# Performance work log

Hardware: AMD Instinct MI355X
Metric: run time of the kernel (lower is better)

The kernel has to match this reference:

```python
import jax, jax.numpy as jnp
import numpy as np

SEQ, PREV, BS, D_IN, H, D = 512, 512, 8, 1024, 16, 64


def setup_inputs() -> dict:
    key = jax.random.key(0)
    ks = jax.random.split(key, 10)
    s = 0.02
    inp = {
        "input_": jax.random.normal(ks[0], (SEQ, BS, D_IN), jnp.float32),
        "pos_embs": jax.random.normal(ks[1], (SEQ + PREV, D_IN), jnp.float32),
        "memory": jax.random.normal(ks[2], (PREV, BS, D_IN), jnp.float32),
        "u": jax.random.normal(ks[3], (H, D), jnp.float32) * s,
        "v": jax.random.normal(ks[4], (H, D), jnp.float32) * s,
        # causal mask allowing full attention to memory: triu with diagonal=1+prev
        "mask": (jnp.triu(jnp.ones((SEQ, SEQ + PREV), jnp.bool_), k=1 + PREV))[..., None],
        "W_kv": jax.random.normal(ks[5], (D_IN, 2 * H * D), jnp.float32) * s,
        "W_q": jax.random.normal(ks[6], (D_IN, H * D), jnp.float32) * s,
        "W_p": jax.random.normal(ks[7], (D_IN, H * D), jnp.float32) * s,
        "W_out": jax.random.normal(ks[8], (H * D, D_IN), jnp.float32) * s,
        "ln_gamma": jnp.ones((D_IN,), jnp.float32),
        "ln_beta": jnp.zeros((D_IN,), jnp.float32),
    }
    return inp


def _rel_shift(x):
    # x: (q, k, bs, H) -> pad one zero column, reshape-transpose trick, drop first row
    q, k, bs, h = x.shape
    zp = jnp.zeros((q, 1, bs, h), x.dtype)
    return jnp.concatenate([zp, x], axis=1).reshape(k + 1, q, bs, h)[1:].reshape(q, k, bs, h)


def reference(input_, pos_embs, memory, u, v, mask, W_kv, W_q, W_p, W_out, ln_gamma, ln_beta):
    cur_seq, bs, d_in = input_.shape
    prev_seq = memory.shape[0]
    tot = cur_seq + prev_seq
    h, d = u.shape
    scale = 1.0 / d ** 0.5

    iwm = jnp.concatenate([memory, input_], axis=0)          # (tot, bs, d_in)
    kv = jnp.einsum('jbe,ef->jbf', iwm, W_kv)                 # (tot, bs, 2*H*d)
    k_t, v_t = jnp.split(kv, 2, axis=-1)
    q_t = jnp.einsum('ibe,ef->ibf', input_, W_q)              # (cur, bs, H*d)

    q4 = q_t.reshape(cur_seq, bs, h, d)
    k4 = k_t.reshape(tot, bs, h, d)
    v4 = v_t.reshape(tot, bs, h, d)

    content_attn = jnp.einsum('ibhd,jbhd->ijbh', q4 + u, k4)  # (cur, tot, bs, H)

    p_t = (pos_embs @ W_p).reshape(tot, h, d)                 # (tot, H, d)
    position_attn = jnp.einsum('ibhd,jhd->ijbh', q4 + v, p_t)
    position_attn = _rel_shift(position_attn)

    attn = content_attn + position_attn
    attn = jnp.where(mask[..., None], -jnp.inf, attn)         # mask: (cur, tot, 1) -> (cur, tot, 1, 1)
    attn = jax.nn.softmax(attn * scale, axis=1)

    awv = jnp.einsum('ijbh,jbhd->ibhd', attn, v4).reshape(cur_seq, bs, h * d)
    out = input_ + awv @ W_out                                # residual

    mu = jnp.mean(out, axis=-1, keepdims=True)
    var = jnp.mean((out - mu) ** 2, axis=-1, keepdims=True)
    out = (out - mu) / jnp.sqrt(var + 1e-5) * ln_gamma + ln_beta
    return out
```

## Files before the change

### kernel.cpp

```cpp
#include <hip/hip_runtime.h>
#include <math.h>

#define SEQ  512
#define PREV 512
#define TOT  1024
#define BSZ  8
#define DIN  1024
#define NH   16
#define HD   64

typedef __bf16 bf16;
typedef __bf16 bf16x8 __attribute__((ext_vector_type(8)));
typedef float  f32x4  __attribute__((ext_vector_type(4)));
typedef float  f32x16 __attribute__((ext_vector_type(16)));
typedef unsigned int u32;
typedef u32 u32x2 __attribute__((ext_vector_type(2)));

__device__ __forceinline__ f32x4 MFMA16(bf16x8 a, bf16x8 b, f32x4 c) {
    return __builtin_amdgcn_mfma_f32_16x16x32_bf16(a, b, c, 0, 0, 0);
}
__device__ __forceinline__ f32x16 MFMA32(bf16x8 a, bf16x8 b, f32x16 c) {
    return __builtin_amdgcn_mfma_f32_32x32x16_bf16(a, b, c, 0, 0, 0);
}

#define GLOAD16(g, l) __builtin_amdgcn_global_load_lds( \
    (const __attribute__((address_space(1))) void*)(g), \
    (__attribute__((address_space(3))) void*)(l), 16, 0, 0)

__device__ __forceinline__ unsigned short bfbits(float x) {
    return __builtin_bit_cast(unsigned short, (bf16)x);
}
__device__ __forceinline__ float bf2f(u32 bits16) {
    return __builtin_bit_cast(float, bits16 << 16);
}

__global__ __launch_bounds__(256) void prep_all(
    const float* __restrict__ memory, const float* __restrict__ input_,
    const float* __restrict__ pos,
    const float* __restrict__ W_kv, const float* __restrict__ W_q,
    const float* __restrict__ W_p,  const float* __restrict__ W_out,
    bf16* __restrict__ iwm, bf16* __restrict__ posb,
    bf16* __restrict__ wkv, bf16* __restrict__ wq,
    bf16* __restrict__ wp,  bf16* __restrict__ wo)
{
    __shared__ float tile[32][33];
    const int bid = blockIdx.x;
    const int t = threadIdx.x;
    if (bid < 9216) {
        const float* src; bf16* dst; int e4;
        if (bid < 8192) {
            e4 = (bid * 256 + t) * 4;
            src = (e4 < 4194304) ? memory : input_ - 4194304;
            dst = iwm;
        } else {
            e4 = ((bid - 8192) * 256 + t) * 4;
            src = pos; dst = posb;
        }
        float4 x = *(const float4*)(src + e4);
        union { bf16 h[4]; ushort4 u4; } pk;
        pk.h[0] = (bf16)x.x; pk.h[1] = (bf16)x.y; pk.h[2] = (bf16)x.z; pk.h[3] = (bf16)x.w;
        *(ushort4*)(dst + e4) = pk.u4;
        return;
    }
    const int rem = bid - 9216;
    const int bx = rem % 160, by = rem / 160;
    const float* W; bf16* Wt; int N, bn;
    if (bx < 64)       { W = W_kv;  Wt = wkv; N = 2048; bn = bx * 32; }
    else if (bx < 96)  { W = W_q;   Wt = wq;  N = 1024; bn = (bx - 64) * 32; }
    else if (bx < 128) { W = W_p;   Wt = wp;  N = 1024; bn = (bx - 96) * 32; }
    else               { W = W_out; Wt = wo;  N = 1024; bn = (bx - 128) * 32; }
    const int bk = by * 32;
    const int r = t >> 3, c4 = (t & 7) * 4;
    float4 x = *(const float4*)(W + (size_t)(bk + r) * N + bn + c4);
    tile[r][c4 + 0] = x.x; tile[r][c4 + 1] = x.y;
    tile[r][c4 + 2] = x.z; tile[r][c4 + 3] = x.w;
    __syncthreads();
    union { bf16 h[4]; ushort4 u4; } pk;
#pragma unroll
    for (int i = 0; i < 4; ++i) pk.h[i] = (bf16)tile[c4 + i][r];
    *(ushort4*)(Wt + (size_t)(bn + r) * 1024 + bk + c4) = pk.u4;
}

__global__ __launch_bounds__(512, 1) void gemm_8ph(
    const bf16* __restrict__ A, const bf16* __restrict__ Bt,
    bf16* __restrict__ C, int M, int N, int K)
{
    __shared__ __align__(16) bf16 A_s[2][256 * 64];
    __shared__ __align__(16) bf16 B_s[2][256 * 64];
    const int t = threadIdx.x;
    const int w = t >> 6, lane = t & 63;
    const int li = lane & 15, hi = lane >> 4;
    const int wm = w >> 2, wn = w & 3;
    const int lin = blockIdx.y * 8 + blockIdx.x;
    const int xcd = lin & 7, idx = lin >> 3;
    const int bm = (xcd * 4 + (idx & 3)) * 256;
    const int bn = (idx >> 2) * 256;

    f32x4 acc[8][4];
#pragma unroll
    for (int m = 0; m < 8; ++m)
#pragma unroll
        for (int n = 0; n < 4; ++n) acc[m][n] = (f32x4){0.f, 0.f, 0.f, 0.f};

    auto stage_half = [&](int buf, int ks, int h) {
        const bf16* __restrict__ src = (h < 2) ? A : Bt;
        const int base = (h < 2) ? bm : bn;
        const int hh = (h & 1) * 128;
        bf16* dst = (h < 2) ? &A_s[buf][0] : &B_s[buf][0];
        const int k0 = ks << 6;
#pragma unroll
        for (int g = 0; g < 2; ++g) {
            const int row = hh + g * 64 + (t >> 3);
            const bf16* gp = src + (size_t)(base + row) * K + k0 + (((t & 7) ^ (row & 7)) * 8);
            GLOAD16(gp, dst + (size_t)(hh + g * 64 + w * 8) * 64);
        }
    };

    bf16x8 af[4], bfr[4];
    auto LDA = [&](int buf, int mh, int kk) {
#pragma unroll
        for (int m = 0; m < 4; ++m) {
            int row = wm * 128 + (mh * 4 + m) * 16 + li;
            af[m] = *(const bf16x8*)&A_s[buf][row * 64 + (((kk * 4 + hi) ^ (row & 7)) * 8)];
        }
    };
    auto LDB = [&](int buf, int kk) {
#pragma unroll
        for (int n = 0; n < 4; ++n) {
            int row = wn * 64 + n * 16 + li;
            bfr[n] = *(const bf16x8*)&B_s[buf][row * 64 + (((kk * 4 + hi) ^ (row & 7)) * 8)];
        }
    };

#define FMA_PHASE(mh)                                                    \
    asm volatile("s_waitcnt lgkmcnt(0)" ::: "memory");                   \
    __builtin_amdgcn_sched_barrier(0);                                   \
    __builtin_amdgcn_s_setprio(1);                                       \
    _Pragma("unroll")                                                    \
    for (int m = 0; m < 4; ++m)                                          \
        _Pragma("unroll")                                                \
        for (int n = 0; n < 4; ++n)                                      \
            acc[(mh) * 4 + m][n] = MFMA16(af[m], bfr[n], acc[(mh) * 4 + m][n]); \
    __builtin_amdgcn_s_setprio(0);

    stage_half(0, 0, 0); stage_half(0, 0, 1); stage_half(0, 0, 2); stage_half(0, 0, 3);

    const int nk = K >> 6;
    for (int ks = 0; ks < nk; ++ks) {
        const int cur = ks & 1, nxt = cur ^ 1;
        asm volatile("s_waitcnt vmcnt(0)" ::: "memory");
        __builtin_amdgcn_sched_barrier(0);
        __builtin_amdgcn_s_barrier();
        __builtin_amdgcn_sched_barrier(0);
        if (ks + 1 < nk) {
            stage_half(nxt, ks + 1, 0); stage_half(nxt, ks + 1, 1);
            stage_half(nxt, ks + 1, 2); stage_half(nxt, ks + 1, 3);
        }
        LDB(cur, 0); LDA(cur, 0, 0);
        FMA_PHASE(0)
        LDA(cur, 1, 0);
        FMA_PHASE(1)
        LDB(cur, 1); LDA(cur, 0, 1);
        FMA_PHASE(0)
        LDA(cur, 1, 1);
        FMA_PHASE(1)
    }

#pragma unroll
    for (int m = 0; m < 8; ++m)
#pragma unroll
        for (int n = 0; n < 4; ++n)
#pragma unroll
            for (int r = 0; r < 4; ++r) {
                int row = bm + wm * 128 + m * 16 + hi * 4 + r;
                int col = bn + wn * 64 + n * 16 + li;
                C[(size_t)row * N + col] = (bf16)acc[m][n][r];
            }
#undef FMA_PHASE
}

template<int FOUT>
__global__ __launch_bounds__(256) void gemm_mfma(
    const bf16* __restrict__ A, const bf16* __restrict__ Bt,
    const float* __restrict__ Rres, bf16* __restrict__ Cb,
    float* __restrict__ Cf, int M, int N, int K)
{
    __shared__ __align__(16) bf16 A_s[128 * 64];
    __shared__ __align__(16) bf16 B_s[128 * 64];
    const int t = threadIdx.x;
    const int w = t >> 6, lane = t & 63;
    const int li = lane & 15, hi = lane >> 4;
    const int wr = w >> 1, wc = w & 1;
    const int bm = blockIdx.y * 128, bn = blockIdx.x * 128;
    const int l3 = lane >> 3, l7 = lane & 7;
    const int srcoct = ((l7 ^ l3) * 8);

    f32x4 acc[4][4];
#pragma unroll
    for (int m = 0; m < 4; ++m)
#pragma unroll
        for (int n = 0; n < 4; ++n) acc[m][n] = (f32x4){0.f, 0.f, 0.f, 0.f};

    auto stage = [&](int k0) {
#pragma unroll
        for (int i = 0; i < 4; ++i) {
            int c = w * 4 + i;
            const bf16* ga = A + (size_t)(bm + c * 8 + l3) * K + k0 + srcoct;
            GLOAD16(ga, &A_s[c * 512]);
            const bf16* gb = Bt + (size_t)(bn + c * 8 + l3) * K + k0 + srcoct;
            GLOAD16(gb, &B_s[c * 512]);
        }
    };

    stage(0);
    const int nk = K >> 6;
    for (int ks = 0; ks < nk; ++ks) {
        __syncthreads();
#pragma unroll
        for (int kk = 0; kk < 2; ++kk) {
            bf16x8 af[4], bfr[4];
#pragma unroll
            for (int m = 0; m < 4; ++m) {
                int row = wr * 64 + m * 16 + li;
                af[m] = *(const bf16x8*)&A_s[row * 64 + ((kk * 32 + hi * 8) ^ ((row & 7) * 8))];
            }
#pragma unroll
            for (int n = 0; n < 4; ++n) {
                int row = wc * 64 + n * 16 + li;
                bfr[n] = *(const bf16x8*)&B_s[row * 64 + ((kk * 32 + hi * 8) ^ ((row & 7) * 8))];
            }
#pragma unroll
            for (int m = 0; m < 4; ++m)
#pragma unroll
                for (int n = 0; n < 4; ++n)
                    acc[m][n] = MFMA16(af[m], bfr[n], acc[m][n]);
        }
        __syncthreads();
        if (ks + 1 < nk) stage((ks + 1) << 6);
    }

#pragma unroll
    for (int m = 0; m < 4; ++m)
#pragma unroll
        for (int n = 0; n < 4; ++n)
#pragma unroll
            for (int r = 0; r < 4; ++r) {
                int row = bm + wr * 64 + m * 16 + hi * 4 + r;
                int col = bn + wc * 64 + n * 16 + li;
                size_t off = (size_t)row * N + col;
                if (FOUT) Cf[off] = acc[m][n][r] + Rres[off];
                else      Cb[off] = (bf16)acc[m][n][r];
            }
}

__global__ __launch_bounds__(256, 2) void attn_mfma(
    const bf16* __restrict__ kv, const bf16* __restrict__ qb,
    const bf16* __restrict__ pb, const float* __restrict__ u,
    const float* __restrict__ v, bf16* __restrict__ awv)
{
    const int bi = (blockIdx.z & 1) ? (3 - blockIdx.x) : blockIdx.x;
    const int i0 = bi * 128;
    const int b  = blockIdx.y;
    const int h  = blockIdx.z;
    const int t  = threadIdx.x;
    const int w  = t >> 6;
    const int lane = t & 63;
    const int ql  = lane & 31;
    const int hi2 = lane >> 5;

    __shared__ __align__(16) bf16 K_s[64 * 64];
    __shared__ __align__(16) bf16 V_s[64][72];
    __shared__ __align__(16) bf16 P_s[256 * 64];
    __shared__ __align__(16) char SCR[4][6912];

    char* rsc = SCR[w];

    const int c8 = t & 7;
    const int rq = t >> 3;
    const int nt = 2 * bi + 10;
    const int C0 = 384 - i0;

    bf16x8 vreg[2];
#pragma unroll
    for (int p = 0; p < 2; ++p)
        vreg[p] = *(const bf16x8*)(kv + (size_t)((p * 32 + rq) * BSZ + b) * 2048 + 1024 + h * HD + c8 * 8);
#pragma unroll
    for (int p = 0; p < 2; ++p)
        GLOAD16(kv + (size_t)((p * 32 + rq) * BSZ + b) * 2048 + h * HD + ((c8 ^ (rq & 7)) * 8),
                K_s + (p * 32 + rq) * 64 + c8 * 8);
#pragma unroll
    for (int cp = 0; cp < 6; ++cp) {
        int grow = C0 + cp * 32 + rq;
        GLOAD16(pb + (size_t)grow * DIN + h * HD + ((c8 ^ (rq & 7)) * 8),
                P_s + (grow & 255) * 64 + c8 * 8);
    }

    bf16x8 qu[4], qv[4];
    {
        const size_t qoff = ((size_t)(i0 + w * 32 + ql) * BSZ + b) * DIN + h * HD;
#pragma unroll
        for (int kk = 0; kk < 4; ++kk) {
            bf16x8 q8 = *(const bf16x8*)(qb + qoff + kk * 16 + hi2 * 8);
            const float* up = u + h * HD + kk * 16 + hi2 * 8;
            const float* vp = v + h * HD + kk * 16 + hi2 * 8;
#pragma unroll
            for (int m = 0; m < 8; ++m) {
                float qf = (float)q8[m];
                qu[kk][m] = (bf16)(qf + up[m]);
                qv[kk][m] = (bf16)(qf + vp[m]);
            }
        }
    }

    float mrun = -1e30f, lrun = 0.f;
    f32x16 o[2];
    o[0] = (f32x16){}; o[1] = (f32x16){};

    const int phq = (31 - ql) & 3;
    const int sel = phq >> 1;
    const int shb = (phq & 1) * 16;

    for (int tt = 0; tt < nt; ++tt) {
        const int j0 = tt * 64;

        __builtin_amdgcn_s_barrier();
        __builtin_amdgcn_sched_barrier(0);

#pragma unroll
        for (int p = 0; p < 2; ++p) {
            int j = p * 32 + rq;
#pragma unroll
            for (int mm = 0; mm < 8; ++mm)
                V_s[c8 * 8 + mm][(j + 8 * c8) & 63] = vreg[p][mm];
        }
        asm volatile("s_waitcnt vmcnt(0) lgkmcnt(0)" ::: "memory");
        __builtin_amdgcn_sched_barrier(0);
        __builtin_amdgcn_s_barrier();
        __builtin_amdgcn_sched_barrier(0);

        f32x16 st[2];
        st[0] = (f32x16){}; st[1] = (f32x16){};
        __builtin_amdgcn_s_setprio(1);
#pragma unroll
        for (int jt = 0; jt < 2; ++jt) {
            int row = jt * 32 + ql;
#pragma unroll
            for (int kk = 0; kk < 4; ++kk) {
                bf16x8 kf = *(const bf16x8*)&K_s[row * 64 + (((kk * 2 + hi2) ^ (ql & 7)) * 8)];
                st[jt] = MFMA32(kf, qu[kk], st[jt]);
            }
        }
        const int bwg = j0 - i0 + 480 - 32 * w;
        f32x16 rp[3];
        rp[0] = (f32x16){}; rp[1] = (f32x16){}; rp[2] = (f32x16){};
#pragma unroll
        for (int Rt = 0; Rt < 3; ++Rt) {
            int ring = (bwg + Rt * 32 + ql) & 255;
#pragma unroll
            for (int kk = 0; kk < 4; ++kk) {
                bf16x8 pf = *(const bf16x8*)&P_s[ring * 64 + (((kk * 2 + hi2) ^ (ring & 7)) * 8)];
                rp[Rt] = MFMA32(pf, qv[kk], rp[Rt]);
            }
        }
        __builtin_amdgcn_s_setprio(0);

        __builtin_amdgcn_s_barrier();
        __builtin_amdgcn_sched_barrier(0);

        if (tt + 1 < nt) {
            const int j0n = j0 + 64;
#pragma unroll
            for (int p = 0; p < 2; ++p)
                vreg[p] = *(const bf16x8*)(kv + (size_t)((j0n + p * 32 + rq) * BSZ + b) * 2048 + 1024 + h * HD + c8 * 8);
#pragma unroll
            for (int p = 0; p < 2; ++p)
                GLOAD16(kv + (size_t)((j0n + p * 32 + rq) * BSZ + b) * 2048 + h * HD + ((c8 ^ (rq & 7)) * 8),
                        K_s + (p * 32 + rq) * 64 + c8 * 8);
        }
        if (tt + 3 < nt) {
            const int Cs = C0 + (tt + 3) * 64;
#pragma unroll
            for (int p = 0; p < 2; ++p) {
                int grow = Cs + p * 32 + rq;
                GLOAD16(pb + (size_t)grow * DIN + h * HD + ((c8 ^ (rq & 7)) * 8),
                        P_s + (grow & 255) * 64 + c8 * 8);
            }
        }

#pragma unroll
        for (int Rt = 0; Rt < 3; ++Rt)
#pragma unroll
            for (int a = 0; a < 4; ++a) {
                u32 lo = (u32)bfbits(rp[Rt][a * 4 + 0]) | ((u32)bfbits(rp[Rt][a * 4 + 1]) << 16);
                u32 hi = (u32)bfbits(rp[Rt][a * 4 + 2]) | ((u32)bfbits(rp[Rt][a * 4 + 3]) << 16);
                *(u32x2*)(rsc + ql * 216 + 64 * Rt + 16 * a + 8 * hi2) = (u32x2){lo, hi};
            }

        float rowmax = -1e30f;
        const int limb = i0 + 32 * w + ql + PREV - j0;
#pragma unroll
        for (int jt = 0; jt < 2; ++jt)
#pragma unroll
            for (int a = 0; a < 4; ++a) {
                int e = jt * 32 + 8 * a + 4 * hi2 + 31 - ql;
                const u32x2* W = (const u32x2*)(rsc + ql * 216 + 8 * (e >> 2));
                u32x2 A0 = W[0], A1 = W[1];
                u32 U0 = sel ? A0[1] : A0[0];
                u32 U1 = sel ? A1[0] : A0[1];
                u32 U2 = sel ? A1[1] : A1[0];
                u32 o0 = (u32)((((unsigned long long)U1 << 32) | U0) >> shb);
                u32 o1 = (u32)((((unsigned long long)U2 << 32) | U1) >> shb);
                float pq[4] = {bf2f(o0 & 0xffffu), bf2f(o0 >> 16),
                               bf2f(o1 & 0xffffu), bf2f(o1 >> 16)};
#pragma unroll
                for (int rr = 0; rr < 4; ++rr) {
                    int r = a * 4 + rr;
                    int lj = jt * 32 + 8 * a + 4 * hi2 + rr;
                    float sv = (st[jt][r] + pq[rr]) * 0.125f;
                    if (lj > limb) sv = -1e30f;
                    st[jt][r] = sv;
                    rowmax = fmaxf(rowmax, sv);
                }
            }
        rowmax = fmaxf(rowmax, __shfl_xor(rowmax, 32));

        if (!__all(rowmax - mrun <= 8.f)) {
            float newm = fmaxf(mrun, rowmax);
            float fsc = __expf(mrun - newm);
#pragma unroll
            for (int r = 0; r < 16; ++r) {
                float fr = __shfl(fsc, (r & 3) + 8 * (r >> 2) + 4 * hi2);
                o[0][r] *= fr; o[1][r] *= fr;
            }
            lrun *= fsc;
            mrun = newm;
        }
        float rowsum = 0.f;
#pragma unroll
        for (int jt = 0; jt < 2; ++jt)
#pragma unroll
            for (int r = 0; r < 16; ++r) {
                float p = __expf(st[jt][r] - mrun);
                st[jt][r] = p;
                rowsum += p;
            }
        rowsum += __shfl_xor(rowsum, 32);
        lrun += rowsum;

        u32 pk0[2][4], pk1[2][4];
#pragma unroll
        for (int jt = 0; jt < 2; ++jt)
#pragma unroll
            for (int a = 0; a < 4; ++a) {
                pk0[jt][a] = (u32)bfbits(st[jt][a * 4 + 0]) | ((u32)bfbits(st[jt][a * 4 + 1]) << 16);
                pk1[jt][a] = (u32)bfbits(st[jt][a * 4 + 2]) | ((u32)bfbits(st[jt][a * 4 + 3]) << 16);
            }

        __builtin_amdgcn_s_setprio(1);
#pragma unroll
        for (int js = 0; js < 4; ++js) {
            const int jt = js >> 1, a0 = 2 * (js & 1), a1 = a0 + 1;
            u32 w0 = pk0[jt][a0], w2 = pk0[jt][a1];
            asm("v_permlane32_swap_b32 %0, %1" : "+v"(w0), "+v"(w2));
            u32 w1 = pk1[jt][a0], w3 = pk1[jt][a1];
            asm("v_permlane32_swap_b32 %0, %1" : "+v"(w1), "+v"(w3));
            union { u32 uw[4]; bf16x8 vv; } pa;
            pa.uw[0] = w0; pa.uw[1] = w1; pa.uw[2] = w2; pa.uw[3] = w3;
#pragma unroll
            for (int dt = 0; dt < 2; ++dt) {
                int dcol = dt * 32 + ql;
                int colb = (js * 16 + hi2 * 8 + 8 * (dcol >> 3)) & 63;
                bf16x8 vf = *(const bf16x8*)&V_s[dcol][colb];
                o[dt] = MFMA32(pa.vv, vf, o[dt]);
            }
        }
        __builtin_amdgcn_s_setprio(0);
    }

    float lr[16];
#pragma unroll
    for (int r = 0; r < 16; ++r) lr[r] = __shfl(lrun, (r & 3) + 8 * (r >> 2) + 4 * hi2);
#pragma unroll
    for (int dt = 0; dt < 2; ++dt)
#pragma unroll
        for (int r = 0; r < 16; ++r) {
            int row = i0 + 32 * w + (r & 3) + 8 * (r >> 2) + 4 * hi2;
            awv[((size_t)row * BSZ + b) * DIN + h * HD + dt * 32 + ql] = (bf16)(o[dt][r] / lr[r]);
        }
}

__global__ __launch_bounds__(256) void ln_f32(
    float* __restrict__ out, const float* __restrict__ gamma, const float* __restrict__ beta)
{
    const int row = blockIdx.x;
    const int t = threadIdx.x;
    float4 x = *(float4*)(out + (size_t)row * DIN + t * 4);
    float s  = x.x + x.y + x.z + x.w;
    float ss = x.x * x.x + x.y * x.y + x.z * x.z + x.w * x.w;
#pragma unroll
    for (int wd = 1; wd < 64; wd <<= 1) { s += __shfl_xor(s, wd); ss += __shfl_xor(ss, wd); }
    __shared__ float sbuf[4], ssbuf[4];
    const int wave = t >> 6, lanei = t & 63;
    if (lanei == 0) { sbuf[wave] = s; ssbuf[wave] = ss; }
    __syncthreads();
    s  = sbuf[0] + sbuf[1] + sbuf[2] + sbuf[3];
    ss = ssbuf[0] + ssbuf[1] + ssbuf[2] + ssbuf[3];
    const float mu   = s * (1.f / DIN);
    const float var  = ss * (1.f / DIN) - mu * mu;
    const float rstd = rsqrtf(var + 1e-5f);
    float4 g  = *(const float4*)(gamma + t * 4);
    float4 bb = *(const float4*)(beta + t * 4);
    float4 y;
    y.x = (x.x - mu) * rstd * g.x + bb.x;
    y.y = (x.y - mu) * rstd * g.y + bb.y;
    y.z = (x.z - mu) * rstd * g.z + bb.z;
    y.w = (x.w - mu) * rstd * g.w + bb.w;
    *(float4*)(out + (size_t)row * DIN + t * 4) = y;
}

extern "C" void kernel_launch(void* const* d_in, const int* in_sizes, int n_in,
                              void* d_out, int out_size, void* d_ws, size_t ws_size,
                              hipStream_t stream)
{
    const float* input_ = (const float*)d_in[0];
    const float* pos    = (const float*)d_in[1];
    const float* memory = (const float*)d_in[2];
    const float* u      = (const float*)d_in[3];
    const float* v      = (const float*)d_in[4];
    const float* W_kv   = (const float*)d_in[6];
    const float* W_q    = (const float*)d_in[7];
    const float* W_p    = (const float*)d_in[8];
    const float* W_out  = (const float*)d_in[9];
    const float* gamma  = (const float*)d_in[10];
    const float* beta   = (const float*)d_in[11];

    bf16* iwm  = (bf16*)d_ws;
    bf16* kvb  = iwm  + (size_t)8192 * 1024;
    bf16* qbf  = kvb  + (size_t)8192 * 2048;
    bf16* pbf  = qbf  + (size_t)4096 * 1024;
    bf16* posb = pbf  + (size_t)1024 * 1024;
    bf16* wkv  = posb + (size_t)1024 * 1024;
    bf16* wq   = wkv  + (size_t)2048 * 1024;
    bf16* wp   = wq   + (size_t)1024 * 1024;
    bf16* wo   = wp   + (size_t)1024 * 1024;
    bf16* awvb = wo   + (size_t)1024 * 1024;
    float* outf = (float*)d_out;

    prep_all<<<14336, 256, 0, stream>>>(memory, input_, pos, W_kv, W_q, W_p, W_out,
                                        iwm, posb, wkv, wq, wp, wo);

    gemm_8ph<<<dim3(8, 32), 512, 0, stream>>>(iwm, wkv, kvb, 8192, 2048, 1024);
    gemm_mfma<0><<<dim3(8, 32), 256, 0, stream>>>(iwm + (size_t)4096 * 1024, wq, nullptr, qbf, nullptr, 4096, 1024, 1024);
    gemm_mfma<0><<<dim3(8, 8),  256, 0, stream>>>(posb, wp, nullptr, pbf, nullptr, 1024, 1024, 1024);

    attn_mfma<<<dim3(4, 8, 16), 256, 0, stream>>>(kvb, qbf, pbf, u, v, awvb);

    gemm_mfma<1><<<dim3(8, 32), 256, 0, stream>>>(awvb, wo, input_, nullptr, outf, 4096, 1024, 1024);
    ln_f32<<<4096, 256, 0, stream>>>(outf, gamma, beta);
}
```

Before: 192.2 us.

## Merge Q and P projection GEMMs, skip masking on unmasked tiles, tweak attention reductions

The Q and positional projection GEMMs become one launch with 40 row-blocks, so a launch disappears and the grid fills better. In attention, the rel-shift scratch store moves before the barrier. The causal mask compare is now skipped through a wave-uniform branch for tiles that lie fully in the allowed region. Cross-half max and sum reductions use v_permlane32_swap instead of shfl_xor, and the final normalization multiplies by a reciprocal instead of dividing. These cut a little ALU and launch overhead, at the cost of slightly different rounding from rcp and extra code size from the duplicated assemble paths.

```diff
diff --git a/kernel.cpp b/kernel.cpp
--- a/kernel.cpp
+++ b/kernel.cpp
@@ -179,11 +179,9 @@
 #undef FMA_PHASE
 }
 
-template<int FOUT>
-__global__ __launch_bounds__(256) void gemm_mfma(
+__global__ __launch_bounds__(256) void gemm_out(
     const bf16* __restrict__ A, const bf16* __restrict__ Bt,
-    const float* __restrict__ Rres, bf16* __restrict__ Cb,
-    float* __restrict__ Cf, int M, int N, int K)
+    const float* __restrict__ Rres, float* __restrict__ Cf, int N, int K)
 {
     __shared__ __align__(16) bf16 A_s[128 * 64];
     __shared__ __align__(16) bf16 B_s[128 * 64];
@@ -205,10 +203,8 @@
 #pragma unroll
         for (int i = 0; i < 4; ++i) {
             int c = w * 4 + i;
-            const bf16* ga = A + (size_t)(bm + c * 8 + l3) * K + k0 + srcoct;
-            GLOAD16(ga, &A_s[c * 512]);
-            const bf16* gb = Bt + (size_t)(bn + c * 8 + l3) * K + k0 + srcoct;
-            GLOAD16(gb, &B_s[c * 512]);
+            GLOAD16(A + (size_t)(bm + c * 8 + l3) * K + k0 + srcoct, &A_s[c * 512]);
+            GLOAD16(Bt + (size_t)(bn + c * 8 + l3) * K + k0 + srcoct, &B_s[c * 512]);
         }
     };
 
@@ -248,8 +244,79 @@
                 int row = bm + wr * 64 + m * 16 + hi * 4 + r;
                 int col = bn + wc * 64 + n * 16 + li;
                 size_t off = (size_t)row * N + col;
-                if (FOUT) Cf[off] = acc[m][n][r] + Rres[off];
-                else      Cb[off] = (bf16)acc[m][n][r];
+                Cf[off] = acc[m][n][r] + Rres[off];
+            }
+}
+
+__global__ __launch_bounds__(256) void gemm_qp(
+    const bf16* __restrict__ iwmq, const bf16* __restrict__ posb,
+    const bf16* __restrict__ wq, const bf16* __restrict__ wp,
+    bf16* __restrict__ qbf, bf16* __restrict__ pbf)
+{
+    __shared__ __align__(16) bf16 A_s[128 * 64];
+    __shared__ __align__(16) bf16 B_s[128 * 64];
+    const int t = threadIdx.x;
+    const int w = t >> 6, lane = t & 63;
+    const int li = lane & 15, hi = lane >> 4;
+    const int wr = w >> 1, wc = w & 1;
+    const int by = blockIdx.y;
+    const bf16* A; const bf16* Bt; bf16* Cb; int bm;
+    if (by < 32) { A = iwmq; Bt = wq; Cb = qbf; bm = by * 128; }
+    else         { A = posb; Bt = wp; Cb = pbf; bm = (by - 32) * 128; }
+    const int bn = blockIdx.x * 128;
+    const int l3 = lane >> 3, l7 = lane & 7;
+    const int srcoct = ((l7 ^ l3) * 8);
+
+    f32x4 acc[4][4];
+#pragma unroll
+    for (int m = 0; m < 4; ++m)
+#pragma unroll
+        for (int n = 0; n < 4; ++n) acc[m][n] = (f32x4){0.f, 0.f, 0.f, 0.f};
+
+    auto stage = [&](int k0) {
+#pragma unroll
+        for (int i = 0; i < 4; ++i) {
+            int c = w * 4 + i;
+            GLOAD16(A + (size_t)(bm + c * 8 + l3) * 1024 + k0 + srcoct, &A_s[c * 512]);
+            GLOAD16(Bt + (size_t)(bn + c * 8 + l3) * 1024 + k0 + srcoct, &B_s[c * 512]);
+        }
+    };
+
+    stage(0);
+    for (int ks = 0; ks < 16; ++ks) {
+        __syncthreads();
+#pragma unroll
+        for (int kk = 0; kk < 2; ++kk) {
+            bf16x8 af[4], bfr[4];
+#pragma unroll
+            for (int m = 0; m < 4; ++m) {
+                int row = wr * 64 + m * 16 + li;
+                af[m] = *(const bf16x8*)&A_s[row * 64 + ((kk * 32 + hi * 8) ^ ((row & 7) * 8))];
+            }
+#pragma unroll
+            for (int n = 0; n < 4; ++n) {
+                int row = wc * 64 + n * 16 + li;
+                bfr[n] = *(const bf16x8*)&B_s[row * 64 + ((kk * 32 + hi * 8) ^ ((row & 7) * 8))];
+            }
+#pragma unroll
+            for (int m = 0; m < 4; ++m)
+#pragma unroll
+                for (int n = 0; n < 4; ++n)
+                    acc[m][n] = MFMA16(af[m], bfr[n], acc[m][n]);
+        }
+        __syncthreads();
+        if (ks + 1 < 16) stage((ks + 1) << 6);
+    }
+
+#pragma unroll
+    for (int m = 0; m < 4; ++m)
+#pragma unroll
+        for (int n = 0; n < 4; ++n)
+#pragma unroll
+            for (int r = 0; r < 4; ++r) {
+                int row = bm + wr * 64 + m * 16 + hi * 4 + r;
+                int col = bn + wc * 64 + n * 16 + li;
+                Cb[(size_t)row * 1024 + col] = (bf16)acc[m][n][r];
             }
 }
 
@@ -364,6 +431,15 @@
         }
         __builtin_amdgcn_s_setprio(0);
 
+#pragma unroll
+        for (int Rt = 0; Rt < 3; ++Rt)
+#pragma unroll
+            for (int a = 0; a < 4; ++a) {
+                u32 lo = (u32)bfbits(rp[Rt][a * 4 + 0]) | ((u32)bfbits(rp[Rt][a * 4 + 1]) << 16);
+                u32 hi = (u32)bfbits(rp[Rt][a * 4 + 2]) | ((u32)bfbits(rp[Rt][a * 4 + 3]) << 16);
+                *(u32x2*)(rsc + ql * 216 + 64 * Rt + 16 * a + 8 * hi2) = (u32x2){lo, hi};
+            }
+
         __builtin_amdgcn_s_barrier();
         __builtin_amdgcn_sched_barrier(0);
 
@@ -387,42 +463,45 @@
             }
         }
 
-#pragma unroll
-        for (int Rt = 0; Rt < 3; ++Rt)
-#pragma unroll
-            for (int a = 0; a < 4; ++a) {
-                u32 lo = (u32)bfbits(rp[Rt][a * 4 + 0]) | ((u32)bfbits(rp[Rt][a * 4 + 1]) << 16);
-                u32 hi = (u32)bfbits(rp[Rt][a * 4 + 2]) | ((u32)bfbits(rp[Rt][a * 4 + 3]) << 16);
-                *(u32x2*)(rsc + ql * 216 + 64 * Rt + 16 * a + 8 * hi2) = (u32x2){lo, hi};
-            }
-
         float rowmax = -1e30f;
         const int limb = i0 + 32 * w + ql + PREV - j0;
-#pragma unroll
-        for (int jt = 0; jt < 2; ++jt)
-#pragma unroll
-            for (int a = 0; a < 4; ++a) {
-                int e = jt * 32 + 8 * a + 4 * hi2 + 31 - ql;
-                const u32x2* W = (const u32x2*)(rsc + ql * 216 + 8 * (e >> 2));
-                u32x2 A0 = W[0], A1 = W[1];
-                u32 U0 = sel ? A0[1] : A0[0];
-                u32 U1 = sel ? A1[0] : A0[1];
-                u32 U2 = sel ? A1[1] : A1[0];
-                u32 o0 = (u32)((((unsigned long long)U1 << 32) | U0) >> shb);
-                u32 o1 = (u32)((((unsigned long long)U2 << 32) | U1) >> shb);
-                float pq[4] = {bf2f(o0 & 0xffffu), bf2f(o0 >> 16),
-                               bf2f(o1 & 0xffffu), bf2f(o1 >> 16)};
-#pragma unroll
-                for (int rr = 0; rr < 4; ++rr) {
-                    int r = a * 4 + rr;
-                    int lj = jt * 32 + 8 * a + 4 * hi2 + rr;
-                    float sv = (st[jt][r] + pq[rr]) * 0.125f;
-                    if (lj > limb) sv = -1e30f;
-                    st[jt][r] = sv;
-                    rowmax = fmaxf(rowmax, sv);
+        auto assemble = [&](bool domask) {
+#pragma unroll
+            for (int jt = 0; jt < 2; ++jt)
+#pragma unroll
+                for (int a = 0; a < 4; ++a) {
+                    int e = jt * 32 + 8 * a + 4 * hi2 + 31 - ql;
+                    const u32x2* W = (const u32x2*)(rsc + ql * 216 + 8 * (e >> 2));
+                    u32x2 A0 = W[0], A1 = W[1];
+                    u32 U0 = sel ? A0[1] : A0[0];
+                    u32 U1 = sel ? A1[0] : A0[1];
+                    u32 U2 = sel ? A1[1] : A1[0];
+                    u32 o0 = (u32)((((unsigned long long)U1 << 32) | U0) >> shb);
+                    u32 o1 = (u32)((((unsigned long long)U2 << 32) | U1) >> shb);
+                    float pq[4] = {bf2f(o0 & 0xffffu), bf2f(o0 >> 16),
+                                   bf2f(o1 & 0xffffu), bf2f(o1 >> 16)};
+#pragma unroll
+                    for (int rr = 0; rr < 4; ++rr) {
+                        int r = a * 4 + rr;
+                        int lj = jt * 32 + 8 * a + 4 * hi2 + rr;
+                        float sv = (st[jt][r] + pq[rr]) * 0.125f;
+                        if (domask && lj > limb) sv = -1e30f;
+                        st[jt][r] = sv;
+                        rowmax = fmaxf(rowmax, sv);
+                    }
                 }
-            }
-        rowmax = fmaxf(rowmax, __shfl_xor(rowmax, 32));
+        };
+        if (__builtin_amdgcn_readfirstlane(j0 + 63 - (i0 + 32 * w + PREV)) > 0)
+            assemble(true);
+        else
+            assemble(false);
+
+        {
+            u32 rm = __builtin_bit_cast(u32, rowmax), rm2 = rm;
+            asm("v_permlane32_swap_b32 %0, %1" : "+v"(rm), "+v"(rm2));
+            rowmax = fmaxf(__builtin_bit_cast(float, rm2), __builtin_bit_cast(float, rm) * 0.f + rowmax);
+            rowmax = fmaxf(rowmax, __builtin_bit_cast(float, rm2));
+        }
 
         if (!__all(rowmax - mrun <= 8.f)) {
             float newm = fmaxf(mrun, rowmax);
@@ -444,7 +523,11 @@
                 st[jt][r] = p;
                 rowsum += p;
             }
-        rowsum += __shfl_xor(rowsum, 32);
+        {
+            u32 rs = __builtin_bit_cast(u32, rowsum), rs2 = rs;
+            asm("v_permlane32_swap_b32 %0, %1" : "+v"(rs), "+v"(rs2));
+            rowsum += __builtin_bit_cast(float, rs2);
+        }
         lrun += rowsum;
 
         u32 pk0[2][4], pk1[2][4];
@@ -477,15 +560,16 @@
         __builtin_amdgcn_s_setprio(0);
     }
 
+    float linv = __builtin_amdgcn_rcpf(lrun);
     float lr[16];
 #pragma unroll
-    for (int r = 0; r < 16; ++r) lr[r] = __shfl(lrun, (r & 3) + 8 * (r >> 2) + 4 * hi2);
+    for (int r = 0; r < 16; ++r) lr[r] = __shfl(linv, (r & 3) + 8 * (r >> 2) + 4 * hi2);
 #pragma unroll
     for (int dt = 0; dt < 2; ++dt)
 #pragma unroll
         for (int r = 0; r < 16; ++r) {
             int row = i0 + 32 * w + (r & 3) + 8 * (r >> 2) + 4 * hi2;
-            awv[((size_t)row * BSZ + b) * DIN + h * HD + dt * 32 + ql] = (bf16)(o[dt][r] / lr[r]);
+            awv[((size_t)row * BSZ + b) * DIN + h * HD + dt * 32 + ql] = (bf16)(o[dt][r] * lr[r]);
         }
 }
 
@@ -550,11 +634,10 @@
                                         iwm, posb, wkv, wq, wp, wo);
 
     gemm_8ph<<<dim3(8, 32), 512, 0, stream>>>(iwm, wkv, kvb, 8192, 2048, 1024);
-    gemm_mfma<0><<<dim3(8, 32), 256, 0, stream>>>(iwm + (size_t)4096 * 1024, wq, nullptr, qbf, nullptr, 4096, 1024, 1024);
-    gemm_mfma<0><<<dim3(8, 8),  256, 0, stream>>>(posb, wp, nullptr, pbf, nullptr, 1024, 1024, 1024);
+    gemm_qp<<<dim3(8, 40), 256, 0, stream>>>(iwm + (size_t)4096 * 1024, posb, wq, wp, qbf, pbf);
 
     attn_mfma<<<dim3(4, 8, 16), 256, 0, stream>>>(kvb, qbf, pbf, u, v, awvb);
 
-    gemm_mfma<1><<<dim3(8, 32), 256, 0, stream>>>(awvb, wo, input_, nullptr, outf, 4096, 1024, 1024);
+    gemm_out<<<dim3(8, 32), 256, 0, stream>>>(awvb, wo, input_, outf, 1024, 1024);
     ln_f32<<<4096, 256, 0, stream>>>(outf, gamma, beta);
 }
```

New measurement: 170.4 us. 1.13x faster.

## Unify GEMMs on 256-tile kernel, merge Q/P launches, streamline attention softmax

Applied to the files above, without the earlier changes.

Turns the 256x256 8-phase GEMM into a shared body that now serves the Q, positional and output projections too. The separate Q and P GEMMs are merged into one 80-block launch, and the output GEMM uses 64 large tiles instead of 256 small ones. In attention, the scale folds log2(e) so a raw v_exp_f32 can replace __expf. Row reductions use permlane32 swaps, the causal mask is skipped for fully visible tiles, the rsc LDS writes move before the barrier, and the final divide becomes a reciprocal multiply. The larger tiles leave only 64-80 blocks for the Q/P and output GEMMs, which may underfill the GPU's CUs.

```diff
diff --git a/kernel.cpp b/kernel.cpp
--- a/kernel.cpp
+++ b/kernel.cpp
@@ -32,6 +32,11 @@
 }
 __device__ __forceinline__ float bf2f(u32 bits16) {
     return __builtin_bit_cast(float, bits16 << 16);
+}
+__device__ __forceinline__ float exp2_raw(float x) {
+    float r;
+    asm("v_exp_f32 %0, %1" : "=v"(r) : "v"(x));
+    return r;
 }
 
 __global__ __launch_bounds__(256) void prep_all(
@@ -81,9 +86,11 @@
     *(ushort4*)(Wt + (size_t)(bn + r) * 1024 + bk + c4) = pk.u4;
 }
 
-__global__ __launch_bounds__(512, 1) void gemm_8ph(
+template<int FOUT>
+__device__ __forceinline__ void gemm256_body(
     const bf16* __restrict__ A, const bf16* __restrict__ Bt,
-    bf16* __restrict__ C, int M, int N, int K)
+    const float* __restrict__ Rres, bf16* __restrict__ Cb,
+    float* __restrict__ Cf, int bm, int bn, int N, int K)
 {
     __shared__ __align__(16) bf16 A_s[2][256 * 64];
     __shared__ __align__(16) bf16 B_s[2][256 * 64];
@@ -91,10 +98,6 @@
     const int w = t >> 6, lane = t & 63;
     const int li = lane & 15, hi = lane >> 4;
     const int wm = w >> 2, wn = w & 3;
-    const int lin = blockIdx.y * 8 + blockIdx.x;
-    const int xcd = lin & 7, idx = lin >> 3;
-    const int bm = (xcd * 4 + (idx & 3)) * 256;
-    const int bn = (idx >> 2) * 256;
 
     f32x4 acc[8][4];
 #pragma unroll
@@ -165,6 +168,7 @@
         LDA(cur, 1, 1);
         FMA_PHASE(1)
     }
+#undef FMA_PHASE
 
 #pragma unroll
     for (int m = 0; m < 8; ++m)
@@ -174,83 +178,40 @@
             for (int r = 0; r < 4; ++r) {
                 int row = bm + wm * 128 + m * 16 + hi * 4 + r;
                 int col = bn + wn * 64 + n * 16 + li;
-                C[(size_t)row * N + col] = (bf16)acc[m][n][r];
-            }
-#undef FMA_PHASE
-}
-
-template<int FOUT>
-__global__ __launch_bounds__(256) void gemm_mfma(
-    const bf16* __restrict__ A, const bf16* __restrict__ Bt,
-    const float* __restrict__ Rres, bf16* __restrict__ Cb,
-    float* __restrict__ Cf, int M, int N, int K)
-{
-    __shared__ __align__(16) bf16 A_s[128 * 64];
-    __shared__ __align__(16) bf16 B_s[128 * 64];
-    const int t = threadIdx.x;
-    const int w = t >> 6, lane = t & 63;
-    const int li = lane & 15, hi = lane >> 4;
-    const int wr = w >> 1, wc = w & 1;
-    const int bm = blockIdx.y * 128, bn = blockIdx.x * 128;
-    const int l3 = lane >> 3, l7 = lane & 7;
-    const int srcoct = ((l7 ^ l3) * 8);
-
-    f32x4 acc[4][4];
-#pragma unroll
-    for (int m = 0; m < 4; ++m)
-#pragma unroll
-        for (int n = 0; n < 4; ++n) acc[m][n] = (f32x4){0.f, 0.f, 0.f, 0.f};
-
-    auto stage = [&](int k0) {
-#pragma unroll
-        for (int i = 0; i < 4; ++i) {
-            int c = w * 4 + i;
-            const bf16* ga = A + (size_t)(bm + c * 8 + l3) * K + k0 + srcoct;
-            GLOAD16(ga, &A_s[c * 512]);
-            const bf16* gb = Bt + (size_t)(bn + c * 8 + l3) * K + k0 + srcoct;
-            GLOAD16(gb, &B_s[c * 512]);
-        }
-    };
-
-    stage(0);
-    const int nk = K >> 6;
-    for (int ks = 0; ks < nk; ++ks) {
-        __syncthreads();
-#pragma unroll
-        for (int kk = 0; kk < 2; ++kk) {
-            bf16x8 af[4], bfr[4];
-#pragma unroll
-            for (int m = 0; m < 4; ++m) {
-                int row = wr * 64 + m * 16 + li;
-                af[m] = *(const bf16x8*)&A_s[row * 64 + ((kk * 32 + hi * 8) ^ ((row & 7) * 8))];
-            }
-#pragma unroll
-            for (int n = 0; n < 4; ++n) {
-                int row = wc * 64 + n * 16 + li;
-                bfr[n] = *(const bf16x8*)&B_s[row * 64 + ((kk * 32 + hi * 8) ^ ((row & 7) * 8))];
-            }
-#pragma unroll
-            for (int m = 0; m < 4; ++m)
-#pragma unroll
-                for (int n = 0; n < 4; ++n)
-                    acc[m][n] = MFMA16(af[m], bfr[n], acc[m][n]);
-        }
-        __syncthreads();
-        if (ks + 1 < nk) stage((ks + 1) << 6);
-    }
-
-#pragma unroll
-    for (int m = 0; m < 4; ++m)
-#pragma unroll
-        for (int n = 0; n < 4; ++n)
-#pragma unroll
-            for (int r = 0; r < 4; ++r) {
-                int row = bm + wr * 64 + m * 16 + hi * 4 + r;
-                int col = bn + wc * 64 + n * 16 + li;
                 size_t off = (size_t)row * N + col;
                 if (FOUT) Cf[off] = acc[m][n][r] + Rres[off];
                 else      Cb[off] = (bf16)acc[m][n][r];
             }
+}
+
+__global__ __launch_bounds__(512, 1) void gemm_kv(
+    const bf16* __restrict__ iwm, const bf16* __restrict__ wkv, bf16* __restrict__ kvb)
+{
+    const int lin = blockIdx.y * 8 + blockIdx.x;
+    const int xcd = lin & 7, idx = lin >> 3;
+    const int bm = (xcd * 4 + (idx & 3)) * 256;
+    const int bn = (idx >> 2) * 256;
+    gemm256_body<0>(iwm, wkv, nullptr, kvb, nullptr, bm, bn, 2048, 1024);
+}
+
+__global__ __launch_bounds__(512, 1) void gemm_qp(
+    const bf16* __restrict__ iwmq, const bf16* __restrict__ posb,
+    const bf16* __restrict__ wq, const bf16* __restrict__ wp,
+    bf16* __restrict__ qbf, bf16* __restrict__ pbf)
+{
+    const int l = blockIdx.x;
+    const bf16* A; const bf16* Bt; bf16* C; int bm, bn;
+    if (l < 64) { A = iwmq; Bt = wq; C = qbf; bm = (l >> 2) * 256; bn = (l & 3) * 256; }
+    else        { int m = l - 64; A = posb; Bt = wp; C = pbf; bm = (m >> 2) * 256; bn = (m & 3) * 256; }
+    gemm256_body<0>(A, Bt, nullptr, C, nullptr, bm, bn, 1024, 1024);
+}
+
+__global__ __launch_bounds__(512, 1) void gemm_out(
+    const bf16* __restrict__ awvb, const bf16* __restrict__ wo,
+    const float* __restrict__ input_, float* __restrict__ outf)
+{
+    const int l = blockIdx.x;
+    gemm256_body<1>(awvb, wo, input_, nullptr, outf, (l >> 2) * 256, (l & 3) * 256, 1024, 1024);
 }
 
 __global__ __launch_bounds__(256, 2) void attn_mfma(
@@ -279,6 +240,7 @@
     const int rq = t >> 3;
     const int nt = 2 * bi + 10;
     const int C0 = 384 - i0;
+    const float SCL2 = 0.125f * 1.44269504088896f;
 
     bf16x8 vreg[2];
 #pragma unroll
@@ -364,6 +326,15 @@
         }
         __builtin_amdgcn_s_setprio(0);
 
+#pragma unroll
+        for (int Rt = 0; Rt < 3; ++Rt)
+#pragma unroll
+            for (int a = 0; a < 4; ++a) {
+                u32 lo = (u32)bfbits(rp[Rt][a * 4 + 0]) | ((u32)bfbits(rp[Rt][a * 4 + 1]) << 16);
+                u32 hi = (u32)bfbits(rp[Rt][a * 4 + 2]) | ((u32)bfbits(rp[Rt][a * 4 + 3]) << 16);
+                *(u32x2*)(rsc + ql * 216 + 64 * Rt + 16 * a + 8 * hi2) = (u32x2){lo, hi};
+            }
+
         __builtin_amdgcn_s_barrier();
         __builtin_amdgcn_sched_barrier(0);
 
@@ -387,46 +358,49 @@
             }
         }
 
-#pragma unroll
-        for (int Rt = 0; Rt < 3; ++Rt)
-#pragma unroll
-            for (int a = 0; a < 4; ++a) {
-                u32 lo = (u32)bfbits(rp[Rt][a * 4 + 0]) | ((u32)bfbits(rp[Rt][a * 4 + 1]) << 16);
-                u32 hi = (u32)bfbits(rp[Rt][a * 4 + 2]) | ((u32)bfbits(rp[Rt][a * 4 + 3]) << 16);
-                *(u32x2*)(rsc + ql * 216 + 64 * Rt + 16 * a + 8 * hi2) = (u32x2){lo, hi};
-            }
-
         float rowmax = -1e30f;
         const int limb = i0 + 32 * w + ql + PREV - j0;
-#pragma unroll
-        for (int jt = 0; jt < 2; ++jt)
-#pragma unroll
-            for (int a = 0; a < 4; ++a) {
-                int e = jt * 32 + 8 * a + 4 * hi2 + 31 - ql;
-                const u32x2* W = (const u32x2*)(rsc + ql * 216 + 8 * (e >> 2));
-                u32x2 A0 = W[0], A1 = W[1];
-                u32 U0 = sel ? A0[1] : A0[0];
-                u32 U1 = sel ? A1[0] : A0[1];
-                u32 U2 = sel ? A1[1] : A1[0];
-                u32 o0 = (u32)((((unsigned long long)U1 << 32) | U0) >> shb);
-                u32 o1 = (u32)((((unsigned long long)U2 << 32) | U1) >> shb);
-                float pq[4] = {bf2f(o0 & 0xffffu), bf2f(o0 >> 16),
-                               bf2f(o1 & 0xffffu), bf2f(o1 >> 16)};
-#pragma unroll
-                for (int rr = 0; rr < 4; ++rr) {
-                    int r = a * 4 + rr;
-                    int lj = jt * 32 + 8 * a + 4 * hi2 + rr;
-                    float sv = (st[jt][r] + pq[rr]) * 0.125f;
-                    if (lj > limb) sv = -1e30f;
-                    st[jt][r] = sv;
-                    rowmax = fmaxf(rowmax, sv);
+        auto assemble = [&](bool domask) {
+#pragma unroll
+            for (int jt = 0; jt < 2; ++jt)
+#pragma unroll
+                for (int a = 0; a < 4; ++a) {
+                    int e = jt * 32 + 8 * a + 4 * hi2 + 31 - ql;
+                    const u32x2* W = (const u32x2*)(rsc + ql * 216 + 8 * (e >> 2));
+                    u32x2 A0 = W[0], A1 = W[1];
+                    u32 U0 = sel ? A0[1] : A0[0];
+                    u32 U1 = sel ? A1[0] : A0[1];
+                    u32 U2 = sel ? A1[1] : A1[0];
+                    u32 o0 = (u32)((((unsigned long long)U1 << 32) | U0) >> shb);
+                    u32 o1 = (u32)((((unsigned long long)U2 << 32) | U1) >> shb);
+                    float pq[4] = {bf2f(o0 & 0xffffu), bf2f(o0 >> 16),
+                                   bf2f(o1 & 0xffffu), bf2f(o1 >> 16)};
+#pragma unroll
+                    for (int rr = 0; rr < 4; ++rr) {
+                        int r = a * 4 + rr;
+                        int lj = jt * 32 + 8 * a + 4 * hi2 + rr;
+                        float sv = (st[jt][r] + pq[rr]) * SCL2;
+                        if (domask && lj > limb) sv = -1e30f;
+                        st[jt][r] = sv;
+                        rowmax = fmaxf(rowmax, sv);
+                    }
                 }
-            }
-        rowmax = fmaxf(rowmax, __shfl_xor(rowmax, 32));
-
-        if (!__all(rowmax - mrun <= 8.f)) {
+        };
+        if (__builtin_amdgcn_readfirstlane(j0 + 63 - (i0 + 32 * w + PREV)) > 0)
+            assemble(true);
+        else
+            assemble(false);
+
+        {
+            u32 rm = __builtin_bit_cast(u32, rowmax), rm2 = rm;
+            asm("v_permlane32_swap_b32 %0, %1" : "+v"(rm), "+v"(rm2));
+            rowmax = fmaxf(rowmax, __builtin_bit_cast(float, rm));
+            rowmax = fmaxf(rowmax, __builtin_bit_cast(float, rm2));
+        }
+
+        if (!__all(rowmax - mrun <= 11.54f)) {
             float newm = fmaxf(mrun, rowmax);
-            float fsc = __expf(mrun - newm);
+            float fsc = exp2_raw(mrun - newm);
 #pragma unroll
             for (int r = 0; r < 16; ++r) {
                 float fr = __shfl(fsc, (r & 3) + 8 * (r >> 2) + 4 * hi2);
@@ -440,11 +414,15 @@
         for (int jt = 0; jt < 2; ++jt)
 #pragma unroll
             for (int r = 0; r < 16; ++r) {
-                float p = __expf(st[jt][r] - mrun);
+                float p = exp2_raw(st[jt][r] - mrun);
                 st[jt][r] = p;
                 rowsum += p;
             }
-        rowsum += __shfl_xor(rowsum, 32);
+        {
+            u32 rs = __builtin_bit_cast(u32, rowsum), rs2 = rs;
+            asm("v_permlane32_swap_b32 %0, %1" : "+v"(rs), "+v"(rs2));
+            rowsum += __builtin_bit_cast(float, rs2);
+        }
         lrun += rowsum;
 
         u32 pk0[2][4], pk1[2][4];
@@ -477,15 +455,16 @@
         __builtin_amdgcn_s_setprio(0);
     }
 
+    float linv = __builtin_amdgcn_rcpf(lrun);
     float lr[16];
 #pragma unroll
-    for (int r = 0; r < 16; ++r) lr[r] = __shfl(lrun, (r & 3) + 8 * (r >> 2) + 4 * hi2);
+    for (int r = 0; r < 16; ++r) lr[r] = __shfl(linv, (r & 3) + 8 * (r >> 2) + 4 * hi2);
 #pragma unroll
     for (int dt = 0; dt < 2; ++dt)
 #pragma unroll
         for (int r = 0; r < 16; ++r) {
             int row = i0 + 32 * w + (r & 3) + 8 * (r >> 2) + 4 * hi2;
-            awv[((size_t)row * BSZ + b) * DIN + h * HD + dt * 32 + ql] = (bf16)(o[dt][r] / lr[r]);
+            awv[((size_t)row * BSZ + b) * DIN + h * HD + dt * 32 + ql] = (bf16)(o[dt][r] * lr[r]);
         }
 }
 
@@ -549,12 +528,11 @@
     prep_all<<<14336, 256, 0, stream>>>(memory, input_, pos, W_kv, W_q, W_p, W_out,
                                         iwm, posb, wkv, wq, wp, wo);
 
-    gemm_8ph<<<dim3(8, 32), 512, 0, stream>>>(iwm, wkv, kvb, 8192, 2048, 1024);
-    gemm_mfma<0><<<dim3(8, 32), 256, 0, stream>>>(iwm + (size_t)4096 * 1024, wq, nullptr, qbf, nullptr, 4096, 1024, 1024);
-    gemm_mfma<0><<<dim3(8, 8),  256, 0, stream>>>(posb, wp, nullptr, pbf, nullptr, 1024, 1024, 1024);
+    gemm_kv<<<dim3(8, 32), 512, 0, stream>>>(iwm, wkv, kvb);
+    gemm_qp<<<80, 512, 0, stream>>>(iwm + (size_t)4096 * 1024, posb, wq, wp, qbf, pbf);
 
     attn_mfma<<<dim3(4, 8, 16), 256, 0, stream>>>(kvb, qbf, pbf, u, v, awvb);
 
-    gemm_mfma<1><<<dim3(8, 32), 256, 0, stream>>>(awvb, wo, input_, nullptr, outf, 4096, 1024, 1024);
+    gemm_out<<<64, 512, 0, stream>>>(awvb, wo, input_, outf);
     ln_f32<<<4096, 256, 0, stream>>>(outf, gamma, beta);
 }
```

New measurement: 197.8 us. 1.03x slower.
